# Performance work log

Measured on AMD Instinct MI355X. Metric: run time of the kernel, lower is better.

Reference implementation:

```python
import jax, jax.numpy as jnp
import numpy as np

NUM_GRAPHS = 64


def setup_inputs() -> dict:
    key = jax.random.key(0)
    ks = jax.random.split(key, 8)
    N, E, D_IN, D_H = 50000, 800000, 128, 256
    x = jax.random.uniform(ks[0], (N, D_IN), dtype=jnp.float32)
    edge_index = jax.random.randint(ks[1], (2, E), 0, N, dtype=jnp.int64)
    batch = jnp.sort(jax.random.randint(ks[2], (N,), 0, NUM_GRAPHS, dtype=jnp.int64))
    s = 1.0 / np.sqrt(D_IN)
    s2 = 1.0 / np.sqrt(D_H)
    W1_rel = jax.random.normal(ks[3], (D_IN, D_H), dtype=jnp.float32) * s
    W1_root = jax.random.normal(ks[4], (D_IN, D_H), dtype=jnp.float32) * s
    b1 = jnp.zeros((D_H,), jnp.float32)
    W2_rel = jax.random.normal(ks[5], (D_H, D_H), dtype=jnp.float32) * s2
    W2_root = jax.random.normal(ks[6], (D_H, D_H), dtype=jnp.float32) * s2
    b2 = jnp.zeros((D_H,), jnp.float32)
    return {"x": x, "edge_index": edge_index, "batch": batch,
            "W1_rel": W1_rel, "W1_root": W1_root, "b1": b1,
            "W2_rel": W2_rel, "W2_root": W2_root, "b2": b2}


def reference(x, edge_index, batch, W1_rel, W1_root, b1, W2_rel, W2_root, b2):
    N = x.shape[0]
    src, dst = edge_index[0], edge_index[1]

    # handcrafted features: per-label fraction of total feature mass + log(graph_size)
    graph_size = jnp.sum(x)
    handcrafted = jnp.concatenate([jnp.sum(x, axis=0) / graph_size,
                                   jnp.log(graph_size)[None]])

    def graph_conv(h, W_rel, W_root, b):
        # PyG GraphConv (aggr='add'): out_i = W_rel @ sum_{j->i} h_j + W_root @ h_i + b
        agg = jax.ops.segment_sum(h[src], dst, num_segments=N)  # [N, d]
        return agg @ W_rel + h @ W_root + b

    h = jax.nn.relu(graph_conv(x, W1_rel, W1_root, b1))
    # layers 2..num_layers share the same weights (module instance reused in original)
    for _ in range(2):
        h = jax.nn.relu(graph_conv(h, W2_rel, W2_root, b2))

    # global_mean_pool over batch ids
    counts = jax.ops.segment_sum(jnp.ones((N,), h.dtype), batch, num_segments=NUM_GRAPHS)
    pooled = jax.ops.segment_sum(h, batch, num_segments=NUM_GRAPHS)
    pooled = pooled / jnp.maximum(counts, 1.0)[:, None]
    return pooled, handcrafted
```

## Files before the change

kernel.cpp:

```cpp
#include <hip/hip_runtime.h>
#include <hip/hip_bf16.h>
#include <string.h>

#define NN 50000
#define NE 800000
#define DIN 128
#define DH 256
#define NG 64
#define PSPLIT 32
#define GCAP 3072

typedef short bf16x8 __attribute__((ext_vector_type(8)));
typedef float f32x4 __attribute__((ext_vector_type(4)));
typedef unsigned int u32x2 __attribute__((ext_vector_type(2)));

__device__ __forceinline__ float bf2f(__hip_bfloat16 v) { return __bfloat162float(v); }
__device__ __forceinline__ float bfbits(unsigned int lo16) {
  unsigned int u = lo16 << 16;
  float f;
  memcpy(&f, &u, 4);
  return f;
}
__device__ __forceinline__ unsigned int packbf2(float x, float y) {
  __hip_bfloat16 bx = __float2bfloat16(x), by = __float2bfloat16(y);
  unsigned short ux, uy;
  memcpy(&ux, &bx, 2);
  memcpy(&uy, &by, 2);
  return (unsigned int)ux | ((unsigned int)uy << 16);
}

__device__ __forceinline__ float loadF(const void* p, long i, int fbf) {
  return fbf ? bf2f(((const __hip_bfloat16*)p)[i]) : ((const float*)p)[i];
}
__device__ __forceinline__ void storeF(void* p, long i, float v, int fbf) {
  if (fbf) ((__hip_bfloat16*)p)[i] = __float2bfloat16(v);
  else ((float*)p)[i] = v;
}
__device__ __forceinline__ int loadI(const void* p, long i, int i64) {
  return i64 ? (int)((const long long*)p)[i] : ((const int*)p)[i];
}

__global__ void k_detect(const void* x, const void* ei, int* flags) {
  __shared__ int s_f32sig, s_i32sig;
  if (threadIdx.x == 0) { s_f32sig = 0; s_i32sig = 0; }
  __syncthreads();
  int t = threadIdx.x;
  const unsigned short* u = (const unsigned short*)x;
  int f = 0;
  for (int i = 2 * t; i < 8192; i += 512) if (u[i] >= 0x4000) f = 1;
  const unsigned int* w = (const unsigned int*)ei;
  int g = 0;
  for (int i = 2 * t + 1; i < 8192; i += 512) if (w[i] != 0u) g = 1;
  if (f) atomicOr(&s_f32sig, 1);
  if (g) atomicOr(&s_i32sig, 1);
  __syncthreads();
  if (t == 0) { flags[0] = s_f32sig ? 0 : 1; flags[1] = s_i32sig ? 0 : 1; }
}

__global__ void k_zero(int* __restrict__ p, int n) {
  int i = blockIdx.x * blockDim.x + threadIdx.x;
  int stride = gridDim.x * blockDim.x;
  for (; i < n; i += stride) p[i] = 0;
}

__global__ __launch_bounds__(256) void k_prep(
    const void* __restrict__ x, __hip_bfloat16* __restrict__ xs,
    float* __restrict__ colsum, const int* __restrict__ flags) {
  int fbf = flags[0];
  int t = threadIdx.x;
  int lane16 = t & 15;
  int rowoff = t >> 4;
  float acc[8] = {};
  for (int r = blockIdx.x * 16 + rowoff; r < NN; r += gridDim.x * 16) {
    uint4 o;
    if (fbf) {
      uint4 v = ((const uint4*)x)[(long)r * 16 + lane16];
      acc[0] += bfbits(v.x & 0xffffu); acc[1] += bfbits(v.x >> 16);
      acc[2] += bfbits(v.y & 0xffffu); acc[3] += bfbits(v.y >> 16);
      acc[4] += bfbits(v.z & 0xffffu); acc[5] += bfbits(v.z >> 16);
      acc[6] += bfbits(v.w & 0xffffu); acc[7] += bfbits(v.w >> 16);
      o = v;
    } else {
      float4 a = ((const float4*)x)[(long)r * 32 + lane16 * 2];
      float4 b = ((const float4*)x)[(long)r * 32 + lane16 * 2 + 1];
      acc[0] += a.x; acc[1] += a.y; acc[2] += a.z; acc[3] += a.w;
      acc[4] += b.x; acc[5] += b.y; acc[6] += b.z; acc[7] += b.w;
      o.x = packbf2(a.x, a.y); o.y = packbf2(a.z, a.w);
      o.z = packbf2(b.x, b.y); o.w = packbf2(b.z, b.w);
    }
    ((uint4*)xs)[((long)(lane16 >> 2) * NN + r) * 4 + (lane16 & 3)] = o;
  }
  __shared__ float s[16][DIN];
#pragma unroll
  for (int k = 0; k < 8; ++k) s[rowoff][lane16 * 8 + k] = acc[k];
  __syncthreads();
  if (t < DIN) {
    float v = 0.f;
#pragma unroll
    for (int ro = 0; ro < 16; ++ro) v += s[ro][t];
    atomicAdd(&colsum[t], v);
  }
}

__global__ void k_handcrafted(const float* __restrict__ colsum, void* __restrict__ out,
                              const int* __restrict__ flags) {
  __shared__ float s[DIN];
  int fbf = flags[0];
  int t = threadIdx.x;
  s[t] = colsum[t];
  __syncthreads();
  for (int off = DIN / 2; off > 0; off >>= 1) {
    if (t < off) s[t] += s[t + off];
    __syncthreads();
  }
  float g = s[0];
  storeF(out, NG * DH + t, colsum[t] / g, fbf);
  if (t == 0) storeF(out, NG * DH + DIN, logf(g), fbf);
}

__global__ void k_pack_w(const void* __restrict__ Wrel, const void* __restrict__ Wroot,
                         const void* __restrict__ bias, __hip_bfloat16* __restrict__ pack,
                         float* __restrict__ biasf, const int* __restrict__ flags, int K) {
  int fbf = flags[0];
  int KS = K >> 5;
  int total = 2 * K * DH;
  int i = blockIdx.x * blockDim.x + threadIdx.x;
  int stride = gridDim.x * blockDim.x;
  for (int p = i; p < total; p += stride) {
    int m = p / (K * DH);
    int r = p % (K * DH);
    int j = r & 7;
    int l = (r >> 3) & 63;
    int q2 = r >> 9;
    int ks = q2 % KS;
    int ct = q2 / KS;
    int kk = ks * 32 + (l >> 4) * 8 + j;
    int col = ct * 16 + (l & 15);
    const void* W = m ? Wroot : Wrel;
    pack[p] = __float2bfloat16(loadF(W, (long)kk * DH + col, fbf));
  }
  if (i < DH) biasf[i] = loadF(bias, i, fbf);
}

__global__ void k_deg(const void* __restrict__ ei, int* __restrict__ cnt,
                      const int* __restrict__ flags) {
  int i64 = flags[1];
  int e = blockIdx.x * blockDim.x + threadIdx.x;
  int stride = gridDim.x * blockDim.x;
  for (; e < NE; e += stride) {
    int d = loadI(ei, (long)NE + e, i64);
    d = min(max(d, 0), NN - 1);
    atomicAdd(&cnt[d], 1);
  }
}

#define SCAN_B 256
__global__ void k_scan1(const int* __restrict__ cnt, int* __restrict__ rowptr,
                        int* __restrict__ bsum) {
  __shared__ int s[SCAN_B];
  int b = blockIdx.x, t = threadIdx.x;
  int i = b * SCAN_B + t;
  int v = (i < NN) ? cnt[i] : 0;
  s[t] = v;
  __syncthreads();
  for (int off = 1; off < SCAN_B; off <<= 1) {
    int xv = (t >= off) ? s[t - off] : 0;
    __syncthreads();
    s[t] += xv;
    __syncthreads();
  }
  if (i < NN) rowptr[i] = s[t] - v;
  if (t == SCAN_B - 1) bsum[b] = s[t];
}

__global__ void k_scan2(int* __restrict__ bsum, int nb) {
  __shared__ int s[SCAN_B];
  int t = threadIdx.x;
  int v = (t < nb) ? bsum[t] : 0;
  s[t] = v;
  __syncthreads();
  for (int off = 1; off < SCAN_B; off <<= 1) {
    int xv = (t >= off) ? s[t - off] : 0;
    __syncthreads();
    s[t] += xv;
    __syncthreads();
  }
  if (t < nb) bsum[t] = s[t] - v;
}

__global__ void k_scan3(int* __restrict__ rowptr, const int* __restrict__ bsum) {
  int i = blockIdx.x * blockDim.x + threadIdx.x;
  int stride = gridDim.x * blockDim.x;
  for (; i < NN; i += stride) rowptr[i] += bsum[i >> 8];
  if (blockIdx.x == 0 && threadIdx.x == 0) rowptr[NN] = NE;
}

__global__ void k_fill(const void* __restrict__ ei, const int* __restrict__ rowptr,
                       int* __restrict__ cur, int* __restrict__ srcs,
                       const int* __restrict__ flags) {
  int i64 = flags[1];
  int e = blockIdx.x * blockDim.x + threadIdx.x;
  int stride = gridDim.x * blockDim.x;
  for (; e < NE; e += stride) {
    int s = loadI(ei, e, i64);
    int d = loadI(ei, (long)NE + e, i64);
    s = min(max(s, 0), NN - 1);
    d = min(max(d, 0), NN - 1);
    int p = atomicAdd(&cur[d], 1);
    srcs[rowptr[d] + p] = s;
  }
}

template <int K>
__global__ __launch_bounds__(256) void k_gathers(
    const int* __restrict__ rowptr, const int* __restrict__ srcs,
    const __hip_bfloat16* __restrict__ hs, __hip_bfloat16* __restrict__ agg) {
  constexpr int SL = K / 32;
  constexpr int HALVES = 8 / SL;
  constexpr int NPH = (NN + HALVES - 1) / HALVES;
  __shared__ int se[GCAP];
  __shared__ int sb[2];
  int role = blockIdx.x & 7;
  int nb = blockIdx.x >> 3;
  int s = role / HALVES;
  int half = role % HALVES;
  int t = threadIdx.x;
  int n0 = half * NPH + nb * 32;
  int nlim = min((half + 1) * NPH, NN);
  if (t == 0) {
    sb[0] = rowptr[n0];
    sb[1] = rowptr[min(n0 + 32, nlim)];
  }
  __syncthreads();
  int wbeg = sb[0];
  int wlen = min(sb[1] - wbeg, GCAP);
  for (int i = t; i < wlen; i += 256)
    se[i] = __builtin_nontemporal_load(&srcs[wbeg + i]);
  __syncthreads();
  int nsub = t >> 3;
  int c = t & 7;
  int node = n0 + nsub;
  if (node >= nlim) return;
  const u32x2* hb = (const u32x2*)hs + (long)s * NN * 8 + c;
  u32x2* agg2 = (u32x2*)agg;
  int beg = rowptr[node], end = rowptr[node + 1];
  float a0 = 0.f, a1 = 0.f, a2 = 0.f, a3 = 0.f;
  if (end - wbeg <= wlen) {
    int ib = beg - wbeg, ie = end - wbeg;
    for (int i = ib; i < ie; i += 8) {
      int idx[8];
      float m[8];
      u32x2 v[8];
#pragma unroll
      for (int u = 0; u < 8; ++u) {
        int j = i + u;
        int ok = j < ie;
        idx[u] = se[ok ? j : ib];
        m[u] = ok ? 1.f : 0.f;
      }
#pragma unroll
      for (int u = 0; u < 8; ++u) v[u] = hb[(long)idx[u] * 8];
#pragma unroll
      for (int u = 0; u < 8; ++u) {
        a0 = fmaf(m[u], bfbits(v[u].x & 0xffffu), a0);
        a1 = fmaf(m[u], bfbits(v[u].x >> 16), a1);
        a2 = fmaf(m[u], bfbits(v[u].y & 0xffffu), a2);
        a3 = fmaf(m[u], bfbits(v[u].y >> 16), a3);
      }
    }
  } else {
    for (int i = beg; i < end; i += 8) {
      int idx[8];
      float m[8];
      u32x2 v[8];
#pragma unroll
      for (int u = 0; u < 8; ++u) {
        int j = i + u;
        int ok = j < end;
        idx[u] = __builtin_nontemporal_load(&srcs[ok ? j : beg]);
        m[u] = ok ? 1.f : 0.f;
      }
#pragma unroll
      for (int u = 0; u < 8; ++u) v[u] = hb[(long)idx[u] * 8];
#pragma unroll
      for (int u = 0; u < 8; ++u) {
        a0 = fmaf(m[u], bfbits(v[u].x & 0xffffu), a0);
        a1 = fmaf(m[u], bfbits(v[u].x >> 16), a1);
        a2 = fmaf(m[u], bfbits(v[u].y & 0xffffu), a2);
        a3 = fmaf(m[u], bfbits(v[u].y >> 16), a3);
      }
    }
  }
  u32x2 o;
  o.x = packbf2(a0, a1);
  o.y = packbf2(a2, a3);
  __builtin_nontemporal_store(o, &agg2[(long)node * (K / 4) + s * 8 + c]);
}

template <int K, bool OUTS>
__global__ __launch_bounds__(256, 4) void k_gemm(
    const __hip_bfloat16* __restrict__ A1, const __hip_bfloat16* __restrict__ A2,
    const __hip_bfloat16* __restrict__ Wpack, const float* __restrict__ bias,
    __hip_bfloat16* __restrict__ out) {
  constexpr int KS = K >> 5;
  int lane = threadIdx.x & 63;
  int wave = threadIdx.x >> 6;
  int m15 = lane & 15;
  int q = lane >> 4;
  int row0 = blockIdx.x * 32;
  const short* A1s = (const short*)A1;
  const short* A2s = (const short*)A2;
  const short* Wp = (const short*)Wpack;
  const int wrootOfs = K * DH;
  f32x4 acc[2][4] = {};
#pragma unroll
  for (int ks = 0; ks < KS; ++ks) {
    int kofs = ks * 32 + q * 8;
    bf16x8 a1[2], a2[2], b1[4], b2[4];
#pragma unroll
    for (int mt = 0; mt < 2; ++mt) {
      int r = row0 + mt * 16 + m15;
      if (r > NN - 1) r = NN - 1;
      a1[mt] = *(const bf16x8*)(A1s + (long)r * K + kofs);
      a2[mt] = *(const bf16x8*)(A2s + ((long)ks * NN + r) * 32 + q * 8);
    }
#pragma unroll
    for (int ct = 0; ct < 4; ++ct) {
      int gct = wave * 4 + ct;
      const short* base = Wp + ((gct * KS + ks) * 64 + lane) * 8;
      b1[ct] = *(const bf16x8*)(base);
      b2[ct] = *(const bf16x8*)(base + wrootOfs);
    }
#pragma unroll
    for (int mt = 0; mt < 2; ++mt)
#pragma unroll
      for (int ct = 0; ct < 4; ++ct) {
        acc[mt][ct] = __builtin_amdgcn_mfma_f32_16x16x32_bf16(a1[mt], b1[ct], acc[mt][ct], 0, 0, 0);
        acc[mt][ct] = __builtin_amdgcn_mfma_f32_16x16x32_bf16(a2[mt], b2[ct], acc[mt][ct], 0, 0, 0);
      }
  }
#pragma unroll
  for (int mt = 0; mt < 2; ++mt)
#pragma unroll
    for (int ct = 0; ct < 4; ++ct) {
      int col = (wave * 4 + ct) * 16 + m15;
      float bv = bias[col];
#pragma unroll
      for (int r = 0; r < 4; ++r) {
        int row = row0 + mt * 16 + q * 4 + r;
        if (row < NN) {
          float v = acc[mt][ct][r] + bv;
          long oidx = OUTS ? (((long)(col >> 5) * NN + row) * 32 + (col & 31))
                           : ((long)row * DH + col);
          out[oidx] = __float2bfloat16(fmaxf(v, 0.f));
        }
      }
    }
}

__global__ void k_bounds(const void* __restrict__ batch, int* __restrict__ gstart,
                         int* __restrict__ gend, const int* __restrict__ flags) {
  int i64 = flags[1];
  int n = blockIdx.x * blockDim.x + threadIdx.x;
  if (n >= NN) return;
  int b = min(max(loadI(batch, n, i64), 0), NG - 1);
  int bp = (n == 0) ? -1 : min(max(loadI(batch, n - 1, i64), 0), NG - 1);
  if (b != bp) gstart[b] = n;
  int bn = (n == NN - 1) ? -1 : min(max(loadI(batch, n + 1, i64), 0), NG - 1);
  if (b != bn) gend[b] = n + 1;
}

__global__ void k_poolpart(const int* __restrict__ gstart, const int* __restrict__ gend,
                           const __hip_bfloat16* __restrict__ h, float* __restrict__ pooled) {
  int g = blockIdx.x;
  int p = blockIdx.y;
  int j = threadIdx.x;
  int s = gstart[g], e = gend[g];
  int len = e - s;
  if (len <= 0) return;
  int chunk = (len + PSPLIT - 1) / PSPLIT;
  int rs = s + p * chunk;
  int re = min(rs + chunk, e);
  if (rs >= re) return;
  const unsigned int* h2 = (const unsigned int*)h;
  float a0 = 0.f, a1 = 0.f;
  for (int r = rs; r < re; ++r) {
    unsigned int v = h2[(long)r * 128 + j];
    a0 += bfbits(v & 0xffffu);
    a1 += bfbits(v >> 16);
  }
  atomicAdd(&pooled[g * DH + 2 * j], a0);
  atomicAdd(&pooled[g * DH + 2 * j + 1], a1);
}

__global__ void k_poolfin(const int* __restrict__ gstart, const int* __restrict__ gend,
                          const float* __restrict__ pooled, void* __restrict__ out,
                          const int* __restrict__ flags) {
  int fbf = flags[0];
  int g = blockIdx.x;
  int j = threadIdx.x;
  float cnt = fmaxf((float)(gend[g] - gstart[g]), 1.0f);
  storeF(out, (long)g * DH + j, pooled[g * DH + j] / cnt, fbf);
}

extern "C" void kernel_launch(void* const* d_in, const int* in_sizes, int n_in,
                              void* d_out, int out_size, void* d_ws, size_t ws_size,
                              hipStream_t stream) {
  const void* x = d_in[0];
  const void* ei = d_in[1];
  const void* batch = d_in[2];
  const void* W1r = d_in[3];
  const void* W1o = d_in[4];
  const void* b1 = d_in[5];
  const void* W2r = d_in[6];
  const void* W2o = d_in[7];
  const void* b2 = d_in[8];
  void* out = d_out;

  char* w = (char*)d_ws;
  auto alloc = [&](size_t bytes) -> char* {
    char* p = w;
    w += (bytes + 255) & ~(size_t)255;
    return p;
  };
  int* flags = (int*)alloc(64);
  const int zero_n = NN + NN + DIN + NG + NG + NG * DH;
  int* zreg = (int*)alloc((size_t)zero_n * 4);
  int* cnt = zreg;
  int* cur = cnt + NN;
  float* colsum = (float*)(cur + NN);
  int* gstart = (int*)(colsum + DIN);
  int* gend = gstart + NG;
  float* pooled = (float*)(gend + NG);
  int* rowptr = (int*)alloc((NN + 1) * 4);
  int* bsum = (int*)alloc(SCAN_B * 4);
  int* srcs = (int*)alloc((size_t)NE * 4);
  __hip_bfloat16* xs = (__hip_bfloat16*)alloc((size_t)NN * DIN * 2);
  __hip_bfloat16* aggb = (__hip_bfloat16*)alloc((size_t)NN * DH * 2);
  __hip_bfloat16* h1s = (__hip_bfloat16*)alloc((size_t)NN * DH * 2);
  __hip_bfloat16* h2s = (__hip_bfloat16*)alloc((size_t)NN * DH * 2);
  __hip_bfloat16* wp1 = (__hip_bfloat16*)alloc((size_t)2 * DIN * DH * 2);
  __hip_bfloat16* wp2 = (__hip_bfloat16*)alloc((size_t)2 * DH * DH * 2);
  float* b1f = (float*)alloc(DH * 4);
  float* b2f = (float*)alloc(DH * 4);
  __hip_bfloat16* hA = h1s;

  const int nblk = (NN + SCAN_B - 1) / SCAN_B;
  const int gemm_grid = (NN + 31) / 32;
  const int g256_grid = 8 * ((NN + 31) / 32);
  const int g128_grid = 8 * ((NN / 2 + 31) / 32);

  k_detect<<<1, 256, 0, stream>>>(x, ei, flags);
  k_zero<<<512, 256, 0, stream>>>(zreg, zero_n);

  k_pack_w<<<64, 256, 0, stream>>>(W1r, W1o, b1, wp1, b1f, flags, DIN);
  k_pack_w<<<128, 256, 0, stream>>>(W2r, W2o, b2, wp2, b2f, flags, DH);
  k_prep<<<1024, 256, 0, stream>>>(x, xs, colsum, flags);
  k_handcrafted<<<1, 128, 0, stream>>>(colsum, out, flags);

  k_deg<<<1024, 256, 0, stream>>>(ei, cnt, flags);
  k_scan1<<<nblk, SCAN_B, 0, stream>>>(cnt, rowptr, bsum);
  k_scan2<<<1, SCAN_B, 0, stream>>>(bsum, nblk);
  k_scan3<<<256, 256, 0, stream>>>(rowptr, bsum);
  k_fill<<<1024, 256, 0, stream>>>(ei, rowptr, cur, srcs, flags);

  k_gathers<DIN><<<g128_grid, 256, 0, stream>>>(rowptr, srcs, xs, aggb);
  k_gemm<DIN, true><<<gemm_grid, 256, 0, stream>>>(aggb, xs, wp1, b1f, h1s);
  k_gathers<DH><<<g256_grid, 256, 0, stream>>>(rowptr, srcs, h1s, aggb);
  k_gemm<DH, true><<<gemm_grid, 256, 0, stream>>>(aggb, h1s, wp2, b2f, h2s);
  k_gathers<DH><<<g256_grid, 256, 0, stream>>>(rowptr, srcs, h2s, aggb);
  k_gemm<DH, false><<<gemm_grid, 256, 0, stream>>>(aggb, h2s, wp2, b2f, hA);

  k_bounds<<<nblk, 256, 0, stream>>>(batch, gstart, gend, flags);
  k_poolpart<<<dim3(NG, PSPLIT), 128, 0, stream>>>(gstart, gend, hA, pooled);
  k_poolfin<<<NG, DH, 0, stream>>>(gstart, gend, pooled, out, flags);
}
```

Before: 516.6 us.

## Split gather edges across two thread groups per node and fuse small kernels

The neighbor gather now gives each node 16 threads instead of 8, processing half as many nodes per block. Two subgroups take alternating 8-edge chunks and combine their partial sums with an xor shuffle before one store. This raises memory-level parallelism for the average degree of about 16, at the cost of more blocks and partly idle lanes on low-degree nodes. Separately, the format-detect kernel is folded into the zeroing kernel and the batch-boundary computation into the rowptr fixup scan, removing two launches. The shared edge cache is also shrunk to match the smaller node tile.

```diff
diff --git a/kernel.cpp b/kernel.cpp
--- a/kernel.cpp
+++ b/kernel.cpp
@@ -8,7 +8,7 @@
 #define DH 256
 #define NG 64
 #define PSPLIT 32
-#define GCAP 3072
+#define GCAP 2048
 
 typedef short bf16x8 __attribute__((ext_vector_type(8)));
 typedef float f32x4 __attribute__((ext_vector_type(4)));
@@ -40,27 +40,27 @@
   return i64 ? (int)((const long long*)p)[i] : ((const int*)p)[i];
 }
 
-__global__ void k_detect(const void* x, const void* ei, int* flags) {
-  __shared__ int s_f32sig, s_i32sig;
-  if (threadIdx.x == 0) { s_f32sig = 0; s_i32sig = 0; }
-  __syncthreads();
-  int t = threadIdx.x;
-  const unsigned short* u = (const unsigned short*)x;
-  int f = 0;
-  for (int i = 2 * t; i < 8192; i += 512) if (u[i] >= 0x4000) f = 1;
-  const unsigned int* w = (const unsigned int*)ei;
-  int g = 0;
-  for (int i = 2 * t + 1; i < 8192; i += 512) if (w[i] != 0u) g = 1;
-  if (f) atomicOr(&s_f32sig, 1);
-  if (g) atomicOr(&s_i32sig, 1);
-  __syncthreads();
-  if (t == 0) { flags[0] = s_f32sig ? 0 : 1; flags[1] = s_i32sig ? 0 : 1; }
-}
-
-__global__ void k_zero(int* __restrict__ p, int n) {
+__global__ void k_zero_detect(int* __restrict__ p, int n, const void* __restrict__ x,
+                              const void* __restrict__ ei, int* __restrict__ flags) {
   int i = blockIdx.x * blockDim.x + threadIdx.x;
   int stride = gridDim.x * blockDim.x;
-  for (; i < n; i += stride) p[i] = 0;
+  for (int k = i; k < n; k += stride) p[k] = 0;
+  if (blockIdx.x == 0) {
+    __shared__ int s_f32sig, s_i32sig;
+    if (threadIdx.x == 0) { s_f32sig = 0; s_i32sig = 0; }
+    __syncthreads();
+    int t = threadIdx.x;
+    const unsigned short* u = (const unsigned short*)x;
+    int f = 0;
+    for (int j = 2 * t; j < 8192; j += 512) if (u[j] >= 0x4000) f = 1;
+    const unsigned int* w = (const unsigned int*)ei;
+    int g = 0;
+    for (int j = 2 * t + 1; j < 8192; j += 512) if (w[j] != 0u) g = 1;
+    if (f) atomicOr(&s_f32sig, 1);
+    if (g) atomicOr(&s_i32sig, 1);
+    __syncthreads();
+    if (t == 0) { flags[0] = s_f32sig ? 0 : 1; flags[1] = s_i32sig ? 0 : 1; }
+  }
 }
 
 __global__ __launch_bounds__(256) void k_prep(
@@ -188,10 +188,20 @@
   if (t < nb) bsum[t] = s[t] - v;
 }
 
-__global__ void k_scan3(int* __restrict__ rowptr, const int* __restrict__ bsum) {
+__global__ void k_scan3b(int* __restrict__ rowptr, const int* __restrict__ bsum,
+                         const void* __restrict__ batch, int* __restrict__ gstart,
+                         int* __restrict__ gend, const int* __restrict__ flags) {
+  int i64 = flags[1];
   int i = blockIdx.x * blockDim.x + threadIdx.x;
   int stride = gridDim.x * blockDim.x;
-  for (; i < NN; i += stride) rowptr[i] += bsum[i >> 8];
+  for (; i < NN; i += stride) {
+    rowptr[i] += bsum[i >> 8];
+    int b = min(max(loadI(batch, i, i64), 0), NG - 1);
+    int bp = (i == 0) ? -1 : min(max(loadI(batch, i - 1, i64), 0), NG - 1);
+    if (b != bp) gstart[b] = i;
+    int bn = (i == NN - 1) ? -1 : min(max(loadI(batch, i + 1, i64), 0), NG - 1);
+    if (b != bn) gend[b] = i + 1;
+  }
   if (blockIdx.x == 0 && threadIdx.x == 0) rowptr[NN] = NE;
 }
 
@@ -218,6 +228,7 @@
   constexpr int SL = K / 32;
   constexpr int HALVES = 8 / SL;
   constexpr int NPH = (NN + HALVES - 1) / HALVES;
+  constexpr int NPB = 16;
   __shared__ int se[GCAP];
   __shared__ int sb[2];
   int role = blockIdx.x & 7;
@@ -225,11 +236,11 @@
   int s = role / HALVES;
   int half = role % HALVES;
   int t = threadIdx.x;
-  int n0 = half * NPH + nb * 32;
+  int n0 = half * NPH + nb * NPB;
   int nlim = min((half + 1) * NPH, NN);
   if (t == 0) {
-    sb[0] = rowptr[n0];
-    sb[1] = rowptr[min(n0 + 32, nlim)];
+    sb[0] = rowptr[min(n0, nlim)];
+    sb[1] = rowptr[min(n0 + NPB, nlim)];
   }
   __syncthreads();
   int wbeg = sb[0];
@@ -237,7 +248,8 @@
   for (int i = t; i < wlen; i += 256)
     se[i] = __builtin_nontemporal_load(&srcs[wbeg + i]);
   __syncthreads();
-  int nsub = t >> 3;
+  int nsub = t >> 4;
+  int sub = (t >> 3) & 1;
   int c = t & 7;
   int node = n0 + nsub;
   if (node >= nlim) return;
@@ -247,7 +259,7 @@
   float a0 = 0.f, a1 = 0.f, a2 = 0.f, a3 = 0.f;
   if (end - wbeg <= wlen) {
     int ib = beg - wbeg, ie = end - wbeg;
-    for (int i = ib; i < ie; i += 8) {
+    for (int i = ib + sub * 8; i < ie; i += 16) {
       int idx[8];
       float m[8];
       u32x2 v[8];
@@ -269,7 +281,7 @@
       }
     }
   } else {
-    for (int i = beg; i < end; i += 8) {
+    for (int i = beg + sub * 8; i < end; i += 16) {
       int idx[8];
       float m[8];
       u32x2 v[8];
@@ -291,10 +303,16 @@
       }
     }
   }
-  u32x2 o;
-  o.x = packbf2(a0, a1);
-  o.y = packbf2(a2, a3);
-  __builtin_nontemporal_store(o, &agg2[(long)node * (K / 4) + s * 8 + c]);
+  a0 += __shfl_xor(a0, 8);
+  a1 += __shfl_xor(a1, 8);
+  a2 += __shfl_xor(a2, 8);
+  a3 += __shfl_xor(a3, 8);
+  if (sub == 0) {
+    u32x2 o;
+    o.x = packbf2(a0, a1);
+    o.y = packbf2(a2, a3);
+    __builtin_nontemporal_store(o, &agg2[(long)node * (K / 4) + s * 8 + c]);
+  }
 }
 
 template <int K, bool OUTS>
@@ -356,18 +374,6 @@
         }
       }
     }
-}
-
-__global__ void k_bounds(const void* __restrict__ batch, int* __restrict__ gstart,
-                         int* __restrict__ gend, const int* __restrict__ flags) {
-  int i64 = flags[1];
-  int n = blockIdx.x * blockDim.x + threadIdx.x;
-  if (n >= NN) return;
-  int b = min(max(loadI(batch, n, i64), 0), NG - 1);
-  int bp = (n == 0) ? -1 : min(max(loadI(batch, n - 1, i64), 0), NG - 1);
-  if (b != bp) gstart[b] = n;
-  int bn = (n == NN - 1) ? -1 : min(max(loadI(batch, n + 1, i64), 0), NG - 1);
-  if (b != bn) gend[b] = n + 1;
 }
 
 __global__ void k_poolpart(const int* __restrict__ gstart, const int* __restrict__ gend,
@@ -447,11 +453,10 @@
 
   const int nblk = (NN + SCAN_B - 1) / SCAN_B;
   const int gemm_grid = (NN + 31) / 32;
-  const int g256_grid = 8 * ((NN + 31) / 32);
-  const int g128_grid = 8 * ((NN / 2 + 31) / 32);
-
-  k_detect<<<1, 256, 0, stream>>>(x, ei, flags);
-  k_zero<<<512, 256, 0, stream>>>(zreg, zero_n);
+  const int g256_grid = 8 * ((NN + 15) / 16);
+  const int g128_grid = 8 * ((NN / 2 + 15) / 16);
+
+  k_zero_detect<<<512, 256, 0, stream>>>(zreg, zero_n, x, ei, flags);
 
   k_pack_w<<<64, 256, 0, stream>>>(W1r, W1o, b1, wp1, b1f, flags, DIN);
   k_pack_w<<<128, 256, 0, stream>>>(W2r, W2o, b2, wp2, b2f, flags, DH);
@@ -461,7 +466,7 @@
   k_deg<<<1024, 256, 0, stream>>>(ei, cnt, flags);
   k_scan1<<<nblk, SCAN_B, 0, stream>>>(cnt, rowptr, bsum);
   k_scan2<<<1, SCAN_B, 0, stream>>>(bsum, nblk);
-  k_scan3<<<256, 256, 0, stream>>>(rowptr, bsum);
+  k_scan3b<<<256, 256, 0, stream>>>(rowptr, bsum, batch, gstart, gend, flags);
   k_fill<<<1024, 256, 0, stream>>>(ei, rowptr, cur, srcs, flags);
 
   k_gathers<DIN><<<g128_grid, 256, 0, stream>>>(rowptr, srcs, xs, aggb);
@@ -471,7 +476,6 @@
   k_gathers<DH><<<g256_grid, 256, 0, stream>>>(rowptr, srcs, h2s, aggb);
   k_gemm<DH, false><<<gemm_grid, 256, 0, stream>>>(aggb, h2s, wp2, b2f, hA);
 
-  k_bounds<<<nblk, 256, 0, stream>>>(batch, gstart, gend, flags);
   k_poolpart<<<dim3(NG, PSPLIT), 128, 0, stream>>>(gstart, gend, hA, pooled);
   k_poolfin<<<NG, DH, 0, stream>>>(gstart, gend, pooled, out, flags);
 }
```

After: 532.5 us. 3.1% more time.
